# Optimization experiments

Hardware: AMD Instinct MI355X
Metric: run time of the kernel (lower is better)

Reference implementation:

```python
import jax, jax.numpy as jnp
import numpy as np

NUM_KERNELS = 21
MAX_KSIZE = 21
INIT_KSIZE = 3
_INCREMENT = (MAX_KSIZE - INIT_KSIZE) / (NUM_KERNELS - 2)
# faithful to: int(init + i*increment // 2 * 2), capped at max
KSIZES = [min(MAX_KSIZE, int(INIT_KSIZE + i * _INCREMENT // 2 * 2)) for i in range(NUM_KERNELS)]
SIGMAS = np.linspace(0.5, 1.0, NUM_KERNELS)


def _gauss_kernel(k, sigma):
    # 1D normalized gaussian, outer product -> 2D kernel summing to 1
    x = np.arange(k, dtype=np.float32)
    g = np.exp(-((x - k // 2) ** 2) / (2.0 * sigma ** 2))
    g = g / g.sum()
    w2d = np.outer(g, g).astype(np.float32)
    # depthwise weight, OIHW with feature_group_count=3 -> (3, 1, k, k)
    return jnp.asarray(np.broadcast_to(w2d, (3, 1, k, k)).copy())


_WEIGHTS = [_gauss_kernel(k, s) for k, s in zip(KSIZES, SIGMAS)]


def setup_inputs() -> dict:
    key = jax.random.key(0)
    x = jax.random.normal(key, (8, 3, 512, 512), dtype=jnp.float32)
    return {"x": x}


def reference(x):
    outs = [x]
    for k, w in zip(KSIZES, _WEIGHTS):
        p = (k - 1) // 2
        xp = jnp.pad(x, ((0, 0), (0, 0), (p, p), (p, p)), mode="reflect")
        y = jax.lax.conv_general_dilated(
            xp, w, window_strides=(1, 1), padding="VALID",
            dimension_numbers=("NCHW", "OIHW", "NCHW"),
            feature_group_count=3,
        )
        outs.append(y)
    # [x, conv_0(x), ..., conv_20(x)] along channels -> (B, 66, H, W)
    return jnp.concatenate(outs, axis=1)
```

## Files before the change

kernel.cpp:

```cpp
#include <hip/hip_runtime.h>
#include <math.h>

#define NK   21
#define TILE 64
#define HALO 4
#define IN_W (TILE + 2*HALO)
#define HW   512

typedef float f32x4 __attribute__((ext_vector_type(4)));

struct GParams {
    float g[NK][5];
    int   R[NK];
};

__device__ __forceinline__ int refl(int v) {
    v = (v < 0) ? -v : v;
    return (v > HW - 1) ? (2 * (HW - 1) - v) : v;
}

template<int R>
__device__ __forceinline__ void vpass(const float* sIn, float* sScr,
                                      const float g[5], int tid) {
    constexpr int WIN = 8 + 2 * R;
    for (int t = tid; t < 8 * IN_W; t += 256) {
        int rg = t / IN_W;
        int c  = t - rg * IN_W;
        const float* src = sIn + (8 * rg + HALO - R) * IN_W + c;
        float win[WIN];
        #pragma unroll
        for (int j = 0; j < WIN; ++j) win[j] = src[j * IN_W];
        float* dst = sScr + (8 * rg) * IN_W + c;
        #pragma unroll
        for (int s = 0; s < 8; ++s) {
            float acc = g[0] * win[s + R];
            #pragma unroll
            for (int d = 1; d <= R; ++d)
                acc += g[d] * (win[s + R - d] + win[s + R + d]);
            dst[s * IN_W] = acc;
        }
    }
}

template<int R>
__device__ __forceinline__ void hpass(const float* sScr, float* op,
                                      const float g[5], int tid, int y0, int x0) {
    for (int t = tid; t < 512; t += 256) {
        int r  = t >> 3;
        int w0 = (t & 7) << 3;
        const f32x4* rp = (const f32x4*)(sScr + r * IN_W + w0);
        f32x4 A = rp[0], B = rp[1], C = rp[2], D = rp[3];
        float win[16] = {A.x, A.y, A.z, A.w, B.x, B.y, B.z, B.w,
                         C.x, C.y, C.z, C.w, D.x, D.y, D.z, D.w};
        float o[8];
        #pragma unroll
        for (int u = 0; u < 8; ++u) {
            float acc = g[0] * win[u + 4];
            #pragma unroll
            for (int d = 1; d <= R; ++d)
                acc += g[d] * (win[u + 4 - d] + win[u + 4 + d]);
            o[u] = acc;
        }
        float* po = op + (y0 + r) * HW + x0 + w0;
        f32x4 v0 = {o[0], o[1], o[2], o[3]};
        f32x4 v1 = {o[4], o[5], o[6], o[7]};
        __builtin_nontemporal_store(v0, (f32x4*)po);
        __builtin_nontemporal_store(v1, (f32x4*)po + 1);
    }
}

__global__ __launch_bounds__(256, 4)
void gauss_all(const float* __restrict__ x, float* __restrict__ out, GParams P) {
    __shared__ float sIn[IN_W * IN_W];
    __shared__ float sScr[TILE * IN_W];
    const int tid   = threadIdx.x;
    const int bid   = blockIdx.x;
    const int plane = bid >> 6;
    const int tile  = bid & 63;
    const int bb = plane / 3, cc = plane - 3 * bb;
    const int y0 = (tile >> 3) << 6;
    const int x0 = (tile & 7) << 6;
    const float* ip = x + (size_t)plane * (HW * HW);

    for (int t = tid; t < IN_W * IN_W; t += 256) {
        int ir = t / IN_W;
        int ic = t - ir * IN_W;
        sIn[t] = ip[refl(y0 - HALO + ir) * HW + refl(x0 - HALO + ic)];
    }
    __syncthreads();

    {
        float* op = out + (size_t)(bb * 66 + cc) * (HW * HW);
        for (int t = tid; t < 1024; t += 256) {
            int r = t >> 4, w4 = (t & 15) << 2;
            f32x4 v = *(const f32x4*)(sIn + (HALO + r) * IN_W + HALO + w4);
            __builtin_nontemporal_store(v, (f32x4*)(op + (y0 + r) * HW + x0 + w4));
        }
    }

    #pragma unroll 1
    for (int i = 0; i < NK; ++i) {
        float g[5];
        #pragma unroll
        for (int d = 0; d < 5; ++d) g[d] = P.g[i][d];
        float* op = out + (size_t)(bb * 66 + 3 + 3 * i + cc) * (HW * HW);
        switch (P.R[i]) {
            case 1: vpass<1>(sIn, sScr, g, tid); __syncthreads();
                    hpass<1>(sScr, op, g, tid, y0, x0); break;
            case 2: vpass<2>(sIn, sScr, g, tid); __syncthreads();
                    hpass<2>(sScr, op, g, tid, y0, x0); break;
            case 3: vpass<3>(sIn, sScr, g, tid); __syncthreads();
                    hpass<3>(sScr, op, g, tid, y0, x0); break;
            default: vpass<4>(sIn, sScr, g, tid); __syncthreads();
                    hpass<4>(sScr, op, g, tid, y0, x0); break;
        }
        __syncthreads();
    }
}

static GParams make_params() {
    GParams P;
    const double inc = 18.0 / 19.0;
    for (int i = 0; i < NK; ++i) {
        double f1 = (double)i * inc;
        double f3 = floor(f1 / 2.0) * 2.0;
        int ks = (int)(3.0 + f3);
        if (ks > 21) ks = 21;
        int p = (ks - 1) / 2;
        double sig = 0.5 + 0.025 * (double)i;
        double s2  = 2.0 * sig * sig;
        double S = 0.0;
        for (int m = -p; m <= p; ++m) S += exp(-(double)(m * m) / s2);
        int R = p;
        for (int r = 1; r <= p; ++r) {
            double Sr = 0.0;
            for (int m = -r; m <= r; ++m) Sr += exp(-(double)(m * m) / s2);
            if ((S - Sr) / S <= 3e-4) { R = r; break; }
        }
        if (R > 4) R = 4;
        P.R[i] = R;
        for (int d = 0; d < 5; ++d)
            P.g[i][d] = (d <= R) ? (float)(exp(-(double)(d * d) / s2) / S) : 0.0f;
    }
    return P;
}

extern "C" void kernel_launch(void* const* d_in, const int* in_sizes, int n_in,
                              void* d_out, int out_size, void* d_ws, size_t ws_size,
                              hipStream_t stream) {
    const float* x = (const float*)d_in[0];
    float* out = (float*)d_out;
    GParams P = make_params();
    gauss_all<<<dim3(24 * 64), dim3(256), 0, stream>>>(x, out, P);
}
```

Baseline: 697.8 us.

## Split Gaussian kernels across separate blocks and vectorize vertical pass

Each tile/plane now launches 22 blocks, one per Gaussian kernel plus one for copying the identity channel, instead of one block looping over all 21 kernels. This greatly increases the number of independent blocks to fill the GPU and removes per-kernel serial loops and barriers, at the cost of reloading the haloed input tile per kernel. The vertical pass is rewritten to operate on float4 columns with a padded scratch row stride.

New measurement: 677.4 us. 1.03x faster.

```diff
diff --git a/kernel.cpp b/kernel.cpp
--- a/kernel.cpp
+++ b/kernel.cpp
@@ -1,11 +1,12 @@
 #include <hip/hip_runtime.h>
 #include <math.h>
 
-#define NK   21
-#define TILE 64
-#define HALO 4
-#define IN_W (TILE + 2*HALO)
-#define HW   512
+#define NK    21
+#define TILE  64
+#define HALO  4
+#define IN_W  72
+#define SCR_W 76
+#define HW    512
 
 typedef float f32x4 __attribute__((ext_vector_type(4)));
 
@@ -22,22 +23,22 @@
 template<int R>
 __device__ __forceinline__ void vpass(const float* sIn, float* sScr,
                                       const float g[5], int tid) {
-    constexpr int WIN = 8 + 2 * R;
-    for (int t = tid; t < 8 * IN_W; t += 256) {
-        int rg = t / IN_W;
-        int c  = t - rg * IN_W;
-        const float* src = sIn + (8 * rg + HALO - R) * IN_W + c;
-        float win[WIN];
+    constexpr int WIN = 4 + 2 * R;
+    for (int t = tid; t < 16 * 18; t += 256) {
+        int rg = t / 18;
+        int cg = t - rg * 18;
+        const f32x4* src = (const f32x4*)(sIn + (4 * rg + HALO - R) * IN_W) + cg;
+        f32x4 win[WIN];
         #pragma unroll
-        for (int j = 0; j < WIN; ++j) win[j] = src[j * IN_W];
-        float* dst = sScr + (8 * rg) * IN_W + c;
+        for (int j = 0; j < WIN; ++j) win[j] = src[j * (IN_W / 4)];
+        f32x4* dst = (f32x4*)(sScr + (4 * rg) * SCR_W) + cg;
         #pragma unroll
-        for (int s = 0; s < 8; ++s) {
-            float acc = g[0] * win[s + R];
+        for (int s = 0; s < 4; ++s) {
+            f32x4 acc = g[0] * win[s + R];
             #pragma unroll
             for (int d = 1; d <= R; ++d)
                 acc += g[d] * (win[s + R - d] + win[s + R + d]);
-            dst[s * IN_W] = acc;
+            dst[s * (SCR_W / 4)] = acc;
         }
     }
 }
@@ -48,7 +49,7 @@
     for (int t = tid; t < 512; t += 256) {
         int r  = t >> 3;
         int w0 = (t & 7) << 3;
-        const f32x4* rp = (const f32x4*)(sScr + r * IN_W + w0);
+        const f32x4* rp = (const f32x4*)(sScr + r * SCR_W + w0);
         f32x4 A = rp[0], B = rp[1], C = rp[2], D = rp[3];
         float win[16] = {A.x, A.y, A.z, A.w, B.x, B.y, B.z, B.w,
                          C.x, C.y, C.z, C.w, D.x, D.y, D.z, D.w};
@@ -72,15 +73,27 @@
 __global__ __launch_bounds__(256, 4)
 void gauss_all(const float* __restrict__ x, float* __restrict__ out, GParams P) {
     __shared__ float sIn[IN_W * IN_W];
-    __shared__ float sScr[TILE * IN_W];
-    const int tid   = threadIdx.x;
-    const int bid   = blockIdx.x;
-    const int plane = bid >> 6;
-    const int tile  = bid & 63;
+    __shared__ float sScr[TILE * SCR_W];
+    const int tid = threadIdx.x;
+    const int bid = blockIdx.x;
+    const int tg  = bid / 22;
+    const int j   = bid - tg * 22;
+    const int plane = tg >> 6;
+    const int tile  = tg & 63;
     const int bb = plane / 3, cc = plane - 3 * bb;
     const int y0 = (tile >> 3) << 6;
     const int x0 = (tile & 7) << 6;
     const float* ip = x + (size_t)plane * (HW * HW);
+
+    if (j == NK) {
+        float* op = out + (size_t)(bb * 66 + cc) * (HW * HW);
+        for (int t = tid; t < 1024; t += 256) {
+            int r = t >> 4, c4 = (t & 15) << 2;
+            f32x4 v = *(const f32x4*)(ip + (y0 + r) * HW + x0 + c4);
+            __builtin_nontemporal_store(v, (f32x4*)(op + (y0 + r) * HW + x0 + c4));
+        }
+        return;
+    }
 
     for (int t = tid; t < IN_W * IN_W; t += 256) {
         int ir = t / IN_W;
@@ -89,32 +102,20 @@
     }
     __syncthreads();
 
-    {
-        float* op = out + (size_t)(bb * 66 + cc) * (HW * HW);
-        for (int t = tid; t < 1024; t += 256) {
-            int r = t >> 4, w4 = (t & 15) << 2;
-            f32x4 v = *(const f32x4*)(sIn + (HALO + r) * IN_W + HALO + w4);
-            __builtin_nontemporal_store(v, (f32x4*)(op + (y0 + r) * HW + x0 + w4));
-        }
-    }
+    float g[5];
+    #pragma unroll
+    for (int d = 0; d < 5; ++d) g[d] = P.g[j][d];
+    float* op = out + (size_t)(bb * 66 + 3 + 3 * j + cc) * (HW * HW);
 
-    #pragma unroll 1
-    for (int i = 0; i < NK; ++i) {
-        float g[5];
-        #pragma unroll
-        for (int d = 0; d < 5; ++d) g[d] = P.g[i][d];
-        float* op = out + (size_t)(bb * 66 + 3 + 3 * i + cc) * (HW * HW);
-        switch (P.R[i]) {
-            case 1: vpass<1>(sIn, sScr, g, tid); __syncthreads();
-                    hpass<1>(sScr, op, g, tid, y0, x0); break;
-            case 2: vpass<2>(sIn, sScr, g, tid); __syncthreads();
-                    hpass<2>(sScr, op, g, tid, y0, x0); break;
-            case 3: vpass<3>(sIn, sScr, g, tid); __syncthreads();
-                    hpass<3>(sScr, op, g, tid, y0, x0); break;
-            default: vpass<4>(sIn, sScr, g, tid); __syncthreads();
-                    hpass<4>(sScr, op, g, tid, y0, x0); break;
-        }
-        __syncthreads();
+    switch (P.R[j]) {
+        case 1: vpass<1>(sIn, sScr, g, tid); __syncthreads();
+                hpass<1>(sScr, op, g, tid, y0, x0); break;
+        case 2: vpass<2>(sIn, sScr, g, tid); __syncthreads();
+                hpass<2>(sScr, op, g, tid, y0, x0); break;
+        case 3: vpass<3>(sIn, sScr, g, tid); __syncthreads();
+                hpass<3>(sScr, op, g, tid, y0, x0); break;
+        default: vpass<4>(sIn, sScr, g, tid); __syncthreads();
+                hpass<4>(sScr, op, g, tid, y0, x0); break;
     }
 }
 
@@ -151,5 +152,5 @@
     const float* x = (const float*)d_in[0];
     float* out = (float*)d_out;
     GParams P = make_params();
-    gauss_all<<<dim3(24 * 64), dim3(256), 0, stream>>>(x, out, P);
+    gauss_all<<<dim3(24 * 64 * 22), dim3(256), 0, stream>>>(x, out, P);
 }
```
